# Performance work log

Hardware: AMD Instinct MI355X
Metric: run time of the kernel (lower is better)

## Reference

```python
import jax, jax.numpy as jnp
import numpy as np

B, C, F, TARGET = 16, 256, 30000, 15000


def setup_inputs() -> dict:
    key = jax.random.key(0)
    k1, k2 = jax.random.split(key)
    fe = jax.random.normal(k1, (B, C, F), dtype=jnp.float32)
    # group assignment produced by the host-side greedy collapse / union-find;
    # modeled as a random surjective-ish map face -> output group
    group_ids = jax.random.randint(k2, (B, F), 0, TARGET, dtype=jnp.int64)
    return {"fe": fe, "group_ids": group_ids}


def reference(fe, group_ids):
    # fe: [B, C, F] float, group_ids: [B, F] int in [0, TARGET)
    # Faithful to MeshUnion.rebuild_features: out = fe @ groups / occurrences,
    # i.e. per-mesh segmented mean of face features into TARGET groups.
    def per_mesh(f, g):
        # f: [C, F], g: [F]
        sums = jax.ops.segment_sum(f.T, g, num_segments=TARGET)          # [TARGET, C]
        counts = jax.ops.segment_sum(jnp.ones((F,), f.dtype), g,
                                     num_segments=TARGET)                 # [TARGET]
        return (sums / jnp.maximum(counts, 1.0)[:, None]).T               # [C, TARGET]

    out = jax.vmap(per_mesh)(fe, group_ids)  # [B, C, TARGET]
    return out
```

## Files before the change

### kernel.cpp

```cpp
#include <hip/hip_runtime.h>

#define BB 16
#define CC 256
#define FF 30000
#define TGT 15000

__global__ __launch_bounds__(256) void count_kernel(const int* __restrict__ gid,
                                                    int* __restrict__ counts) {
    const int f = blockIdx.x * 256 + threadIdx.x;
    const int b = blockIdx.y;
    if (f < FF) {
        const int g = gid[b * FF + f];
        atomicAdd(&counts[b * TGT + g], 1);
    }
}

__global__ __launch_bounds__(512, 4) void pool_kernel(const float* __restrict__ fe,
                                                      const int* __restrict__ gid,
                                                      const int* __restrict__ counts,
                                                      float* __restrict__ out) {
    __shared__ __align__(16) float smem[TGT];

    const int tid = threadIdx.x;
    const int c = blockIdx.x;
    const int b = blockIdx.y;

    float4* smem4 = reinterpret_cast<float4*>(smem);
    #pragma unroll 2
    for (int i = tid; i < TGT / 4; i += 512) {
        smem4[i] = make_float4(0.f, 0.f, 0.f, 0.f);
    }
    __syncthreads();

    const float4* fe4 = reinterpret_cast<const float4*>(fe + ((size_t)b * CC + c) * FF);
    const int4*   g4  = reinterpret_cast<const int4*>(gid + (size_t)b * FF);

    for (int i = tid; i < FF / 4; i += 512) {
        const float4 v = fe4[i];
        const int4   g = g4[i];
        atomicAdd(&smem[g.x], v.x);
        atomicAdd(&smem[g.y], v.y);
        atomicAdd(&smem[g.z], v.z);
        atomicAdd(&smem[g.w], v.w);
    }
    __syncthreads();

    const int4* cnt4 = reinterpret_cast<const int4*>(counts + (size_t)b * TGT);
    float4* out4 = reinterpret_cast<float4*>(out + ((size_t)b * CC + c) * TGT);

    for (int i = tid; i < TGT / 4; i += 512) {
        const float4 s = smem4[i];
        const int4   n = cnt4[i];
        float4 r;
        r.x = s.x / fmaxf((float)n.x, 1.f);
        r.y = s.y / fmaxf((float)n.y, 1.f);
        r.z = s.z / fmaxf((float)n.z, 1.f);
        r.w = s.w / fmaxf((float)n.w, 1.f);
        out4[i] = r;
    }
}

extern "C" void kernel_launch(void* const* d_in, const int* in_sizes, int n_in,
                              void* d_out, int out_size, void* d_ws, size_t ws_size,
                              hipStream_t stream) {
    const float* fe  = (const float*)d_in[0];
    const int*   gid = (const int*)d_in[1];
    float* out = (float*)d_out;
    int* counts = (int*)d_ws;

    hipMemsetAsync(counts, 0, (size_t)BB * TGT * sizeof(int), stream);

    dim3 cgrid((FF + 255) / 256, BB);
    count_kernel<<<cgrid, 256, 0, stream>>>(gid, counts);

    dim3 pgrid(CC, BB);
    pool_kernel<<<pgrid, 512, 0, stream>>>(fe, gid, counts, out);
}
```

Baseline: 1.169 ms.

## Replace shared-memory atomic pooling with CSR gather via counting sort

Builds a per-mesh CSR layout (scan of group counts, then a scatter that produces a face permutation) so the pool kernel can stage each fe row in LDS and gather-sum each group's faces without atomics. This removes the LDS float atomics in the main kernel. In exchange it adds two small kernels, a 120KB LDS footprint per block that limits occupancy to one block per CU, divergent variable-length loops, and global reads of perm and offs.

```diff
diff --git a/kernel.cpp b/kernel.cpp
--- a/kernel.cpp
+++ b/kernel.cpp
@@ -4,6 +4,8 @@
 #define CC 256
 #define FF 30000
 #define TGT 15000
+#define OSTR 15004
+
 
 __global__ __launch_bounds__(256) void count_kernel(const int* __restrict__ gid,
                                                     int* __restrict__ counts) {
@@ -15,47 +17,93 @@
     }
 }
 
-__global__ __launch_bounds__(512, 4) void pool_kernel(const float* __restrict__ fe,
-                                                      const int* __restrict__ gid,
-                                                      const int* __restrict__ counts,
-                                                      float* __restrict__ out) {
-    __shared__ __align__(16) float smem[TGT];
+__global__ __launch_bounds__(1024) void scan_kernel(const int* __restrict__ counts,
+                                                    int* __restrict__ offs,
+                                                    int* __restrict__ cursor) {
+    const int b = blockIdx.x;
+    const int t = threadIdx.x;
+    const int PER = 15;
+    __shared__ int part[1024];
+
+    int local[PER];
+    int s = 0;
+    const int base = t * PER;
+    #pragma unroll
+    for (int i = 0; i < PER; ++i) {
+        const int g = base + i;
+        const int c = (g < TGT) ? counts[b * TGT + g] : 0;
+        local[i] = c;
+        s += c;
+    }
+    part[t] = s;
+    __syncthreads();
+
+    for (int off = 1; off < 1024; off <<= 1) {
+        const int v = (t >= off) ? part[t - off] : 0;
+        __syncthreads();
+        part[t] += v;
+        __syncthreads();
+    }
+    int run = (t == 0) ? 0 : part[t - 1];
+
+    #pragma unroll
+    for (int i = 0; i < PER; ++i) {
+        const int g = base + i;
+        if (g < TGT) {
+            offs[b * OSTR + g] = run;
+            cursor[b * TGT + g] = run;
+            run += local[i];
+        }
+    }
+    if (t == 1023) offs[b * OSTR + TGT] = FF;
+}
+
+__global__ __launch_bounds__(256) void scatter_kernel(const int* __restrict__ gid,
+                                                      int* __restrict__ cursor,
+                                                      int* __restrict__ perm) {
+    const int f = blockIdx.x * 256 + threadIdx.x;
+    const int b = blockIdx.y;
+    if (f < FF) {
+        const int g = gid[b * FF + f];
+        const int pos = atomicAdd(&cursor[b * TGT + g], 1);
+        perm[b * FF + pos] = f;
+    }
+}
+
+__global__ __launch_bounds__(1024) void pool_kernel(const float* __restrict__ fe,
+                                                    const int* __restrict__ offs,
+                                                    const int* __restrict__ perm,
+                                                    float* __restrict__ out) {
+    __shared__ __align__(16) float row[FF];
 
     const int tid = threadIdx.x;
     const int c = blockIdx.x;
     const int b = blockIdx.y;
 
-    float4* smem4 = reinterpret_cast<float4*>(smem);
-    #pragma unroll 2
-    for (int i = tid; i < TGT / 4; i += 512) {
-        smem4[i] = make_float4(0.f, 0.f, 0.f, 0.f);
+    const float4* fe4 = reinterpret_cast<const float4*>(fe + ((size_t)b * CC + c) * FF);
+    float4* row4 = reinterpret_cast<float4*>(row);
+    for (int i = tid; i < FF / 4; i += 1024) {
+        row4[i] = fe4[i];
     }
     __syncthreads();
 
-    const float4* fe4 = reinterpret_cast<const float4*>(fe + ((size_t)b * CC + c) * FF);
-    const int4*   g4  = reinterpret_cast<const int4*>(gid + (size_t)b * FF);
-
-    for (int i = tid; i < FF / 4; i += 512) {
-        const float4 v = fe4[i];
-        const int4   g = g4[i];
-        atomicAdd(&smem[g.x], v.x);
-        atomicAdd(&smem[g.y], v.y);
-        atomicAdd(&smem[g.z], v.z);
-        atomicAdd(&smem[g.w], v.w);
-    }
-    __syncthreads();
-
-    const int4* cnt4 = reinterpret_cast<const int4*>(counts + (size_t)b * TGT);
+    const int* ob = offs + b * OSTR;
+    const int* pb = perm + (size_t)b * FF;
     float4* out4 = reinterpret_cast<float4*>(out + ((size_t)b * CC + c) * TGT);
 
-    for (int i = tid; i < TGT / 4; i += 512) {
-        const float4 s = smem4[i];
-        const int4   n = cnt4[i];
+    for (int i = tid; i < TGT / 4; i += 1024) {
+        const int4 o = reinterpret_cast<const int4*>(ob)[i];
+        const int e4 = ob[4 * i + 4];
+        float s0 = 0.f, s1 = 0.f, s2 = 0.f, s3 = 0.f;
+        for (int j = o.x; j < o.y; ++j) s0 += row[pb[j]];
+        for (int j = o.y; j < o.z; ++j) s1 += row[pb[j]];
+        for (int j = o.z; j < o.w; ++j) s2 += row[pb[j]];
+        for (int j = o.w; j < e4;  ++j) s3 += row[pb[j]];
         float4 r;
-        r.x = s.x / fmaxf((float)n.x, 1.f);
-        r.y = s.y / fmaxf((float)n.y, 1.f);
-        r.z = s.z / fmaxf((float)n.z, 1.f);
-        r.w = s.w / fmaxf((float)n.w, 1.f);
+        r.x = s0 / fmaxf((float)(o.y - o.x), 1.f);
+        r.y = s1 / fmaxf((float)(o.z - o.y), 1.f);
+        r.z = s2 / fmaxf((float)(o.w - o.z), 1.f);
+        r.w = s3 / fmaxf((float)(e4 - o.w), 1.f);
         out4[i] = r;
     }
 }
@@ -66,13 +114,20 @@
     const float* fe  = (const float*)d_in[0];
     const int*   gid = (const int*)d_in[1];
     float* out = (float*)d_out;
-    int* counts = (int*)d_ws;
+
+    int* ws      = (int*)d_ws;
+    int* counts  = ws;
+    int* offs    = ws + 240000;
+    int* cursor  = ws + 480064;
+    int* perm    = ws + 720064;
 
     hipMemsetAsync(counts, 0, (size_t)BB * TGT * sizeof(int), stream);
 
-    dim3 cgrid((FF + 255) / 256, BB);
-    count_kernel<<<cgrid, 256, 0, stream>>>(gid, counts);
+    dim3 fgrid((FF + 255) / 256, BB);
+    count_kernel<<<fgrid, 256, 0, stream>>>(gid, counts);
+    scan_kernel<<<dim3(BB), 1024, 0, stream>>>(counts, offs, cursor);
+    scatter_kernel<<<fgrid, 256, 0, stream>>>(gid, cursor, perm);
 
     dim3 pgrid(CC, BB);
-    pool_kernel<<<pgrid, 512, 0, stream>>>(fe, gid, counts, out);
+    pool_kernel<<<pgrid, 1024, 0, stream>>>(fe, offs, perm, out);
 }
```

After: 985.9 us. -15.7%, faster.
